# Optimization experiments

Measured on AMD Instinct MI355X. Metric: run time of the kernel, lower is better.

The kernel has to match this reference:

```python
import jax, jax.numpy as jnp
import numpy as np

HEADS = 4
ATTN_MODE = 'strided'
LOCAL_ATTN_CTX = 32
BLOCKSIZE = 32


def strided_transpose(x, n_ctx, local_attn_ctx):
    # [n, t, e] -> [n, bT_ctx, local, e] -> [n, local, bT_ctx, e] -> [n, t, e]
    bT_ctx = n_ctx // local_attn_ctx
    n, t, e = x.shape
    x = x.reshape(n, bT_ctx, local_attn_ctx, e)
    x = jnp.transpose(x, (0, 2, 1, 3))
    return x.reshape(n, t, e)


def setup_inputs() -> dict:
    key = jax.random.key(0)
    kq, kk, kv = jax.random.split(key, 3)
    shape = (2, 4096, 1024)
    return {
        'q': jax.random.normal(kq, shape, dtype=jnp.float32),
        'k': jax.random.normal(kk, shape, dtype=jnp.float32),
        'v': jax.random.normal(kv, shape, dtype=jnp.float32),
    }


def reference(q, k, v):
    n_ctx = q.shape[1]
    if ATTN_MODE == 'strided':
        bT_ctx = n_ctx // LOCAL_ATTN_CTX
        assert bT_ctx % BLOCKSIZE == 0
        q = strided_transpose(q, n_ctx, LOCAL_ATTN_CTX)
        k = strided_transpose(k, n_ctx, LOCAL_ATTN_CTX)
        v = strided_transpose(v, n_ctx, LOCAL_ATTN_CTX)
    n_state = q.shape[-1] // HEADS
    scale = 1.0 / np.sqrt(n_state)
    w = jnp.einsum('nte,nse->nts', q, k)            # [n, t, t] full scores
    w = jax.nn.softmax(w * scale, axis=-1)
    a = jnp.einsum('nts,nse->nte', w, v)
    if ATTN_MODE == 'strided':
        n, t, e = a.shape
        bT_ctx = n_ctx // LOCAL_ATTN_CTX
        a = a.reshape(n, LOCAL_ATTN_CTX, bT_ctx, e)
        a = jnp.transpose(a, (0, 2, 1, 3))
        a = a.reshape(n, t, e)
    return a
```

## Files before the change

kernel.cpp:

```cpp
#include <hip/hip_runtime.h>

using short8  = __attribute__((ext_vector_type(8))) short;
using ushort8 = __attribute__((ext_vector_type(8))) unsigned short;
using f32x4   = __attribute__((ext_vector_type(4))) float;

#define T 4096
#define E 1024
#define NB 2
#define BM 128
#define BN 128
#define BK 32
#define TILE_ELEMS (BM * BK)
#define TILE_A_W   (256 * BK)

__device__ __forceinline__ unsigned short f2bf(float f) {
    unsigned int u = __builtin_bit_cast(unsigned int, f);
    u = (u + 0x7FFFu + ((u >> 16) & 1u)) >> 16;
    return (unsigned short)u;
}

__device__ __forceinline__ void gld16(const unsigned short* g, unsigned short* l) {
    __builtin_amdgcn_global_load_lds(
        (__attribute__((address_space(1))) void*)g,
        (__attribute__((address_space(3))) void*)l, 16, 0, 0);
}

__device__ __forceinline__ void do_cvt(const float* __restrict__ src,
                                       unsigned short* __restrict__ dst, int blk) {
    size_t i = ((size_t)blk * 256 + threadIdx.x) * 8;
    float4 f0 = *(const float4*)(src + i);
    float4 f1 = *(const float4*)(src + i + 4);
    ushort8 u;
    u[0]=f2bf(f0.x); u[1]=f2bf(f0.y); u[2]=f2bf(f0.z); u[3]=f2bf(f0.w);
    u[4]=f2bf(f1.x); u[5]=f2bf(f1.y); u[6]=f2bf(f1.z); u[7]=f2bf(f1.w);
    *(ushort8*)(dst + i) = u;
}

__device__ __forceinline__ void do_vt(const float* __restrict__ v,
                                      unsigned short* __restrict__ vt, int id,
                                      float (*tile)[65]) {
    int b   = id / (64 * 16);
    int rem = id % (64 * 16);
    int t0  = (rem / 16) * 64;
    int e0  = (rem % 16) * 64;
    int tid = threadIdx.x;
    int r   = tid >> 2;
    int c0  = (tid & 3) * 16;
    const float* src = v + ((size_t)(b * T + t0 + r)) * E + e0 + c0;
    #pragma unroll
    for (int i = 0; i < 4; i++) {
        float4 f = *(const float4*)(src + i * 4);
        tile[r][c0 + i*4 + 0] = f.x;
        tile[r][c0 + i*4 + 1] = f.y;
        tile[r][c0 + i*4 + 2] = f.z;
        tile[r][c0 + i*4 + 3] = f.w;
    }
    __syncthreads();
    int er = tid >> 2;
    #pragma unroll
    for (int ch = 0; ch < 2; ch++) {
        int tl = (tid & 3) * 16 + ch * 8;
        ushort8 u;
        #pragma unroll
        for (int j = 0; j < 8; j++) u[j] = f2bf(tile[tl + j][er]);
        *(ushort8*)(vt + ((size_t)(b * E + e0 + er)) * T + t0 + tl) = u;
    }
}

__global__ __launch_bounds__(256) void prep(const float* __restrict__ q,
                                            const float* __restrict__ k,
                                            const float* __restrict__ v,
                                            unsigned short* __restrict__ qb,
                                            unsigned short* __restrict__ kb,
                                            unsigned short* __restrict__ vt,
                                            float* __restrict__ lsum) {
    __shared__ float tile[64][65];
    int bid = blockIdx.x;
    if (bid < 4096)        do_cvt(q, qb, bid);
    else if (bid < 8192)   do_cvt(k, kb, bid - 4096);
    else if (bid < 10240)  do_vt(v, vt, bid - 8192, tile);
    else                   lsum[(bid - 10240) * 256 + threadIdx.x] = 0.0f;
}

__global__ __launch_bounds__(256) void prologue(const float* __restrict__ q,
                                                const float* __restrict__ k,
                                                unsigned short* __restrict__ qb,
                                                unsigned short* __restrict__ kb,
                                                float* __restrict__ lsum) {
    int bid = blockIdx.x;
    if (bid < 4096)      do_cvt(q, qb, bid);
    else if (bid < 8192) do_cvt(k, kb, bid - 4096);
    else                 lsum[(bid - 8192) * 256 + threadIdx.x] = 0.0f;
}
__global__ __launch_bounds__(256) void v_transpose(const float* __restrict__ v,
                                                   unsigned short* __restrict__ vt) {
    __shared__ float tile[64][65];
    do_vt(v, vt, blockIdx.x, tile);
}

template <int KITERS>
__device__ __forceinline__ void gemm_core64(const unsigned short* Abase, int apitch,
                                            const unsigned short* Bbase, int bpitch,
                                            unsigned short* ldsA, unsigned short* ldsB,
                                            int tid, f32x4 (&acc)[4][4]) {
    constexpr int TILE64 = 128 * 64;
    const int lane = tid & 63, wave = tid >> 6;
    const int l15 = lane & 15, kq = lane >> 4;
    const int wm = (wave & 1) * 64, wn = (wave >> 1) * 64;

    int goA[4], goB[4], lo[4];
    #pragma unroll
    for (int i = 0; i < 4; i++) {
        int p = i * 256 + tid;
        int r = p >> 3, s = p & 7;
        int sw = s ^ (r & 7);
        goA[i] = r * apitch + sw * 8;
        goB[i] = r * bpitch + sw * 8;
        lo[i] = (i * 256 + wave * 64) * 8;
    }
    int aoff[2][4], boff[2][4];
    #pragma unroll
    for (int mi = 0; mi < 4; mi++) {
        int r = wm + mi * 16 + l15;
        aoff[0][mi] = (r * 8 + (kq ^ (r & 7))) * 8;
        aoff[1][mi] = (r * 8 + ((kq ^ 4) ^ (r & 7))) * 8;
        int rn = wn + mi * 16 + l15;
        boff[0][mi] = (rn * 8 + (kq ^ (rn & 7))) * 8;
        boff[1][mi] = (rn * 8 + ((kq ^ 4) ^ (rn & 7))) * 8;
    }

    #pragma unroll
    for (int i = 0; i < 4; i++) gld16(Abase + goA[i], ldsA + lo[i]);
    #pragma unroll
    for (int i = 0; i < 4; i++) gld16(Bbase + goB[i], ldsB + lo[i]);

    int cbuf = 0;
    for (int kt = 0; kt < KITERS; kt++) {
        int pk = (kt + 1 < KITERS) ? (kt + 1) : 0;
        int ob = cbuf ^ 1;
        asm volatile("s_barrier" ::: "memory");
        #pragma unroll
        for (int i = 0; i < 4; i++) gld16(Abase + goA[i] + pk * 64, ldsA + ob * TILE64 + lo[i]);
        #pragma unroll
        for (int i = 0; i < 4; i++) gld16(Bbase + goB[i] + pk * 64, ldsB + ob * TILE64 + lo[i]);
        asm volatile("s_waitcnt vmcnt(8)" ::: "memory");
        asm volatile("s_barrier" ::: "memory");

        const unsigned short* A = ldsA + cbuf * TILE64;
        const unsigned short* B = ldsB + cbuf * TILE64;
        #pragma unroll
        for (int ks = 0; ks < 2; ks++) {
            short8 af[4], bf[4];
            #pragma unroll
            for (int i = 0; i < 4; i++) {
                af[i] = *(const short8*)(A + aoff[ks][i]);
                bf[i] = *(const short8*)(B + boff[ks][i]);
            }
            #pragma unroll
            for (int mi = 0; mi < 4; mi++)
                #pragma unroll
                for (int ni = 0; ni < 4; ni++)
                    acc[mi][ni] = __builtin_amdgcn_mfma_f32_16x16x32_bf16(af[mi], bf[ni], acc[mi][ni], 0, 0, 0);
        }
        cbuf = ob;
    }
}

template <int KITERS>
__device__ __forceinline__ void gemm_core_wide(const unsigned short* Abase, int apitch,
                                               const unsigned short* Bbase, int bpitch,
                                               unsigned short* ldsA, unsigned short* ldsB,
                                               int tid, f32x4 (&acc)[4][4]) {
    const int lane = tid & 63, wave = tid >> 6;
    const int l15 = lane & 15, kq = lane >> 4;
    const int wm = (wave & 3) * 64, wn = (wave >> 2) * 64;

    const unsigned short* ga[2];
    int lao[2];
    #pragma unroll
    for (int i = 0; i < 2; i++) {
        int p = i * 512 + tid;
        int r = p >> 2;
        int kqw = (p & 3) ^ ((p >> 3) & 3);
        ga[i] = Abase + (size_t)r * apitch + kqw * 8;
        lao[i] = (i * 512 + wave * 64) * 8;
    }
    const unsigned short* gb;
    int lbo;
    {
        int p = tid;
        int r = p >> 2;
        int kqw = (p & 3) ^ ((p >> 3) & 3);
        gb = Bbase + (size_t)r * bpitch + kqw * 8;
        lbo = (wave * 64) * 8;
    }
    int aoff[4], boff[4];
    #pragma unroll
    for (int mi = 0; mi < 4; mi++) {
        int r = wm + mi * 16 + l15;
        aoff[mi] = (r * 4 + (kq ^ ((r >> 1) & 3))) * 8;
        int rn = wn + mi * 16 + l15;
        boff[mi] = (rn * 4 + (kq ^ ((rn >> 1) & 3))) * 8;
    }

    gld16(ga[0], ldsA + lao[0]);
    gld16(ga[1], ldsA + lao[1]);
    gld16(gb,    ldsB + lbo);

    int cbuf = 0;
    for (int kt = 0; kt < KITERS; kt++) {
        int nxt = (kt + 1 < KITERS) ? (kt + 1) : 0;
        int obuf = cbuf ^ 1;
        asm volatile("s_barrier" ::: "memory");
        gld16(ga[0] + nxt * BK, ldsA + obuf * TILE_A_W + lao[0]);
        gld16(ga[1] + nxt * BK, ldsA + obuf * TILE_A_W + lao[1]);
        gld16(gb    + nxt * BK, ldsB + obuf * TILE_ELEMS + lbo);
        asm volatile("s_waitcnt vmcnt(3)" ::: "memory");
        asm volatile("s_barrier" ::: "memory");

        const unsigned short* A = ldsA + cbuf * TILE_A_W;
        const unsigned short* B = ldsB + cbuf * TILE_ELEMS;
        short8 af[4], bf[4];
        #pragma unroll
        for (int i = 0; i < 4; i++) {
            af[i] = *(const short8*)(A + aoff[i]);
            bf[i] = *(const short8*)(B + boff[i]);
        }
        #pragma unroll
        for (int mi = 0; mi < 4; mi++)
            #pragma unroll
            for (int ni = 0; ni < 4; ni++)
                acc[mi][ni] = __builtin_amdgcn_mfma_f32_16x16x32_bf16(af[mi], bf[ni], acc[mi][ni], 0, 0, 0);

        cbuf = obuf;
    }
}

__global__ __launch_bounds__(512, 2) void pass1(const unsigned short* __restrict__ qb,
                                                const unsigned short* __restrict__ kb,
                                                unsigned short* __restrict__ P,
                                                float* __restrict__ lsum) {
    __shared__ unsigned short ldsA[2 * TILE_A_W];
    __shared__ unsigned short ldsB[2 * TILE_ELEMS];
    const int bx = blockIdx.x;
    const int x = bx & 7, j = bx >> 3;
    const int gm = x * 4 + (j & 3);
    const int nt = j >> 2;
    const int b = gm >> 4, mt = gm & 15;
    const int tid = threadIdx.x;

    f32x4 acc[4][4];
    #pragma unroll
    for (int i = 0; i < 4; i++)
        #pragma unroll
        for (int jj = 0; jj < 4; jj++) acc[i][jj] = {};

    gemm_core_wide<E / BK>(qb + ((size_t)b * T + mt * 256) * E, E,
                           kb + ((size_t)b * T + nt * BN) * E, E,
                           ldsA, ldsB, tid, acc);

    const int lane = tid & 63, wave = tid >> 6;
    const int wm = (wave & 3) * 64, wn = (wave >> 2) * 64;
    const int quad = lane >> 4, l15 = lane & 15;
    const float sl2 = 0.0625f * 1.44269504089f;
    const int col0 = nt * BN + wn + l15;

    #pragma unroll
    for (int mi = 0; mi < 4; mi++) {
        #pragma unroll
        for (int r = 0; r < 4; r++) {
            int row = mt * 256 + wm + mi * 16 + quad * 4 + r;
            size_t base = ((size_t)b * T + row) * T + col0;
            float s = 0.0f;
            #pragma unroll
            for (int ni = 0; ni < 4; ni++) {
                float p = exp2f(acc[mi][ni][r] * sl2 - 12.0f);
                P[base + ni * 16] = f2bf(p);
                s += p;
            }
            s += __shfl_xor(s, 1);
            s += __shfl_xor(s, 2);
            s += __shfl_xor(s, 4);
            s += __shfl_xor(s, 8);
            if (l15 == 0) atomicAdd(lsum + b * T + row, s);
        }
    }
}

__global__ __launch_bounds__(256, 2) void pass2(const unsigned short* __restrict__ P,
                                                const unsigned short* __restrict__ vt,
                                                const float* __restrict__ lsum,
                                                float* __restrict__ out) {
    constexpr int TILE64 = 128 * 64;
    __shared__ unsigned short ldsA[2 * TILE64];
    __shared__ unsigned short ldsB[2 * TILE64];

    const int bx = blockIdx.x;
    const int x = bx & 7, j = bx >> 3;
    const int gm = x * 8 + (j & 7);
    const int nt = j >> 3;
    const int b = gm >> 5, mt = gm & 31;
    const int tid = threadIdx.x;

    f32x4 acc[4][4];
    #pragma unroll
    for (int i = 0; i < 4; i++)
        #pragma unroll
        for (int jj = 0; jj < 4; jj++) acc[i][jj] = {};

    gemm_core64<T / 64>(P + ((size_t)b * T + mt * 128) * T, T,
                        vt + ((size_t)b * E + nt * 128) * T, T,
                        ldsA, ldsB, tid, acc);

    const int lane = tid & 63, wave = tid >> 6;
    const int wm = (wave & 1) * 64, wn = (wave >> 1) * 64;
    const int quad = lane >> 4, l15 = lane & 15;
    const int col0 = nt * 128 + wn + l15;

    #pragma unroll
    for (int mi = 0; mi < 4; mi++) {
        #pragma unroll
        for (int r = 0; r < 4; r++) {
            int row = mt * 128 + wm + mi * 16 + quad * 4 + r;
            float rl = 1.0f / lsum[b * T + row];
            size_t base = ((size_t)b * T + row) * E + col0;
            #pragma unroll
            for (int ni = 0; ni < 4; ni++)
                out[base + ni * 16] = acc[mi][ni][r] * rl;
        }
    }
}

extern "C" void kernel_launch(void* const* d_in, const int* in_sizes, int n_in,
                              void* d_out, int out_size, void* d_ws, size_t ws_size,
                              hipStream_t stream) {
    const float* q = (const float*)d_in[0];
    const float* k = (const float*)d_in[1];
    const float* v = (const float*)d_in[2];
    float* out = (float*)d_out;

    const size_t QK = (size_t)NB * T * E;
    const size_t PSZ = (size_t)NB * T * T;
    float* lsum = (float*)d_ws;
    unsigned short* qbw = (unsigned short*)((char*)d_ws + 32768);
    unsigned short* kbw = qbw + QK;
    unsigned short* Pw  = kbw + QK;

    const size_t full_need = 32768 + (3 * QK + PSZ) * sizeof(unsigned short);

    if (ws_size >= full_need) {
        unsigned short* vtw = Pw + PSZ;
        prep<<<10272, 256, 0, stream>>>(q, k, v, qbw, kbw, vtw, lsum);
        pass1<<<1024, 512, 0, stream>>>(qbw, kbw, Pw, lsum);
        pass2<<<512, 256, 0, stream>>>(Pw, vtw, lsum, out);
    } else {
        unsigned short* vtw = qbw;
        prologue<<<8224, 256, 0, stream>>>(q, k, qbw, kbw, lsum);
        pass1<<<1024, 512, 0, stream>>>(qbw, kbw, Pw, lsum);
        v_transpose<<<NB * 64 * 16, 256, 0, stream>>>(v, vtw);
        pass2<<<512, 256, 0, stream>>>(Pw, vtw, lsum, out);
    }
}
```

Measured before the change: 286.8 us.

## Fold V transpose into pass1 as extra tail blocks to overlap with GEMM

Removes the combined prep kernel and instead launches the Q/K conversion prologue, then appends 1024 extra blocks to pass1 that each transpose two V tiles into bf16 using the shared LDS buffer. The aim is to hide the memory-bound V transpose behind the compute-bound QK^T GEMM tail. The transpose blocks inherit pass1's 512-thread, large-LDS configuration and are scheduled after the GEMM blocks, so overlap may be limited to the tail.

```diff
diff --git a/kernel.cpp b/kernel.cpp
--- a/kernel.cpp
+++ b/kernel.cpp
@@ -38,12 +38,11 @@
 
 __device__ __forceinline__ void do_vt(const float* __restrict__ v,
                                       unsigned short* __restrict__ vt, int id,
-                                      float (*tile)[65]) {
+                                      float (*tile)[65], int tid) {
     int b   = id / (64 * 16);
     int rem = id % (64 * 16);
     int t0  = (rem / 16) * 64;
     int e0  = (rem % 16) * 64;
-    int tid = threadIdx.x;
     int r   = tid >> 2;
     int c0  = (tid & 3) * 16;
     const float* src = v + ((size_t)(b * T + t0 + r)) * E + e0 + c0;
@@ -65,21 +64,6 @@
         for (int j = 0; j < 8; j++) u[j] = f2bf(tile[tl + j][er]);
         *(ushort8*)(vt + ((size_t)(b * E + e0 + er)) * T + t0 + tl) = u;
     }
-}
-
-__global__ __launch_bounds__(256) void prep(const float* __restrict__ q,
-                                            const float* __restrict__ k,
-                                            const float* __restrict__ v,
-                                            unsigned short* __restrict__ qb,
-                                            unsigned short* __restrict__ kb,
-                                            unsigned short* __restrict__ vt,
-                                            float* __restrict__ lsum) {
-    __shared__ float tile[64][65];
-    int bid = blockIdx.x;
-    if (bid < 4096)        do_cvt(q, qb, bid);
-    else if (bid < 8192)   do_cvt(k, kb, bid - 4096);
-    else if (bid < 10240)  do_vt(v, vt, bid - 8192, tile);
-    else                   lsum[(bid - 10240) * 256 + threadIdx.x] = 0.0f;
 }
 
 __global__ __launch_bounds__(256) void prologue(const float* __restrict__ q,
@@ -95,7 +79,7 @@
 __global__ __launch_bounds__(256) void v_transpose(const float* __restrict__ v,
                                                    unsigned short* __restrict__ vt) {
     __shared__ float tile[64][65];
-    do_vt(v, vt, blockIdx.x, tile);
+    do_vt(v, vt, blockIdx.x, tile, threadIdx.x);
 }
 
 template <int KITERS>
@@ -112,8 +96,8 @@
     #pragma unroll
     for (int i = 0; i < 4; i++) {
         int p = i * 256 + tid;
-        int r = p >> 3, s = p & 7;
-        int sw = s ^ (r & 7);
+        int r = p >> 3, c = p & 7;
+        int sw = c ^ (r & 7);
         goA[i] = r * apitch + sw * 8;
         goB[i] = r * bpitch + sw * 8;
         lo[i] = (i * 256 + wave * 64) * 8;
@@ -238,16 +222,29 @@
 
 __global__ __launch_bounds__(512, 2) void pass1(const unsigned short* __restrict__ qb,
                                                 const unsigned short* __restrict__ kb,
+                                                const float* __restrict__ v,
+                                                unsigned short* __restrict__ vt,
                                                 unsigned short* __restrict__ P,
                                                 float* __restrict__ lsum) {
-    __shared__ unsigned short ldsA[2 * TILE_A_W];
-    __shared__ unsigned short ldsB[2 * TILE_ELEMS];
+    __shared__ unsigned short lds[2 * TILE_A_W + 2 * TILE_ELEMS];
     const int bx = blockIdx.x;
+    const int tid = threadIdx.x;
+
+    if (bx >= 1024) {
+        const int vb = bx - 1024;
+        float (*tileA)[65] = (float (*)[65])lds;
+        float (*tileB)[65] = (float (*)[65])(lds + 8320);
+        if (tid < 256) do_vt(v, vt, vb * 2,     tileA, tid);
+        else           do_vt(v, vt, vb * 2 + 1, tileB, tid - 256);
+        return;
+    }
+
+    unsigned short* ldsA = lds;
+    unsigned short* ldsB = lds + 2 * TILE_A_W;
     const int x = bx & 7, j = bx >> 3;
     const int gm = x * 4 + (j & 3);
     const int nt = j >> 2;
     const int b = gm >> 4, mt = gm & 15;
-    const int tid = threadIdx.x;
 
     f32x4 acc[4][4];
     #pragma unroll
@@ -350,13 +347,13 @@
 
     if (ws_size >= full_need) {
         unsigned short* vtw = Pw + PSZ;
-        prep<<<10272, 256, 0, stream>>>(q, k, v, qbw, kbw, vtw, lsum);
-        pass1<<<1024, 512, 0, stream>>>(qbw, kbw, Pw, lsum);
+        prologue<<<8224, 256, 0, stream>>>(q, k, qbw, kbw, lsum);
+        pass1<<<1024 + 1024, 512, 0, stream>>>(qbw, kbw, v, vtw, Pw, lsum);
         pass2<<<512, 256, 0, stream>>>(Pw, vtw, lsum, out);
     } else {
         unsigned short* vtw = qbw;
         prologue<<<8224, 256, 0, stream>>>(q, k, qbw, kbw, lsum);
-        pass1<<<1024, 512, 0, stream>>>(qbw, kbw, Pw, lsum);
+        pass1<<<1024, 512, 0, stream>>>(qbw, kbw, v, vtw, Pw, lsum);
         v_transpose<<<NB * 64 * 16, 256, 0, stream>>>(v, vtw);
         pass2<<<512, 256, 0, stream>>>(Pw, vtw, lsum, out);
     }
```

Measured after the change: 284.3 us. No clear change (-0.9%).
